# Kernel tuning notes

Hardware: AMD Instinct MI355X
Metric: run time of the kernel (lower is better)

## Reference

```python
import jax, jax.numpy as jnp
import numpy as np

B, T, E, H = 8, 1024, 1024, 16
HD = E // H  # head dim = 64
HID = 4 * E  # mlp hidden (stretch=4)
EPS = 1e-5


def setup_inputs() -> dict:
    key = jax.random.key(0)
    ks = jax.random.split(key, 8)
    s = lambda fan_in: 1.0 / np.sqrt(fan_in)
    return {
        "x": jax.random.normal(ks[0], (B, T, E), jnp.float32),
        # LayerNorm 1 (pre-attention)
        "ln1_g": jnp.ones((E,), jnp.float32),
        "ln1_b": jnp.zeros((E,), jnp.float32),
        # attention qkv + output proj (stored [in, out])
        "Wqkv": jax.random.normal(ks[1], (E, 3 * E), jnp.float32) * s(E),
        "bqkv": jnp.zeros((3 * E,), jnp.float32),
        "Wproj": jax.random.normal(ks[2], (E, E), jnp.float32) * s(E),
        "bproj": jnp.zeros((E,), jnp.float32),
        # LayerNorm 2 (pre-MLP)
        "ln2_g": jnp.ones((E,), jnp.float32),
        "ln2_b": jnp.zeros((E,), jnp.float32),
        # MLP: E -> 4E -> E with GELU
        "Wfc": jax.random.normal(ks[3], (E, HID), jnp.float32) * s(E),
        "bfc": jnp.zeros((HID,), jnp.float32),
        "Wout": jax.random.normal(ks[4], (HID, E), jnp.float32) * s(HID),
        "bout": jnp.zeros((E,), jnp.float32),
    }


def _layernorm(x, g, b):
    mu = jnp.mean(x, axis=-1, keepdims=True)
    var = jnp.mean(jnp.square(x - mu), axis=-1, keepdims=True)
    return (x - mu) * jax.lax.rsqrt(var + EPS) * g + b


def _attention(x, Wqkv, bqkv, Wproj, bproj):
    qkv = x @ Wqkv + bqkv                       # [B,T,3E]
    q, k, v = jnp.split(qkv, 3, axis=-1)
    # [B,T,E] -> [B,H,T,HD]
    rs = lambda t: t.reshape(B, T, H, HD).transpose(0, 2, 1, 3)
    q, k, v = rs(q), rs(k), rs(v)
    att = jnp.einsum("bhqd,bhkd->bhqk", q, k) * (1.0 / np.sqrt(HD))
    att = jax.nn.softmax(att, axis=-1)          # non-causal (BERT-style)
    y = jnp.einsum("bhqk,bhkd->bhqd", att, v)
    y = y.transpose(0, 2, 1, 3).reshape(B, T, E)
    return y @ Wproj + bproj


def reference(x, ln1_g, ln1_b, Wqkv, bqkv, Wproj, bproj,
              ln2_g, ln2_b, Wfc, bfc, Wout, bout):
    # res=1 => plain residual (w_att = w_mlp = 1.0); drop=0 => dropout identity
    x = x + _attention(_layernorm(x, ln1_g, ln1_b), Wqkv, bqkv, Wproj, bproj)
    h = _layernorm(x, ln2_g, ln2_b)
    x = x + (jax.nn.gelu(h @ Wfc + bfc) @ Wout + bout)
    return x
```

## Files before the change

kernel.cpp:

```cpp
#include <hip/hip_runtime.h>
#include <hip/hip_bf16.h>
#include <hip/hip_fp16.h>

#define B_   8
#define T_   1024
#define E_   1024
#define H_   16
#define HD_  64
#define HID_ 4096

typedef __attribute__((ext_vector_type(8))) _Float16 half8;
typedef __attribute__((ext_vector_type(4))) _Float16 half4;
typedef __attribute__((ext_vector_type(4))) float floatx4;

__device__ __forceinline__ float ld_in(const void* p, size_t i, int mode) {
    if (mode == 0) return ((const float*)p)[i];
    if (mode == 1) return (float)((const __hip_bfloat16*)p)[i];
    return (float)((const _Float16*)p)[i];
}
__device__ __forceinline__ void st_out(void* p, size_t i, int mode, float v) {
    if (mode == 0)      ((float*)p)[i] = v;
    else if (mode == 1) ((__hip_bfloat16*)p)[i] = (__hip_bfloat16)v;
    else                ((_Float16*)p)[i] = (_Float16)v;
}

__device__ __forceinline__ float gelu_f(float v) {
    return 0.5f * v * (1.0f + tanhf(0.7978845608028654f * (v + 0.044715f * v * v * v)));
}

__device__ __forceinline__ void gload_lds16(const void* g, void* l) {
    __builtin_amdgcn_global_load_lds(
        (const __attribute__((address_space(1))) void*)g,
        (__attribute__((address_space(3))) void*)l, 16, 0, 0);
}

__device__ __forceinline__ int xcd_remap(int orig, int nwg) {
    const int xcd = orig & 7, loc = orig >> 3;
    const int nq = nwg >> 3, rr = nwg & 7;
    return (xcd < rr ? xcd * (nq + 1) : rr * (nq + 1) + (xcd - rr) * nq) + loc;
}

__global__ void probe_mode(const void* __restrict__ g, int* __restrict__ mode) {
    if (threadIdx.x == 0) {
        unsigned u = *(const unsigned*)g;
        *mode = (u == 0x3F800000u) ? 0 : 1;
    }
}

__global__ __launch_bounds__(1024) void transpose_cvt(
    const void* __restrict__ in, _Float16* __restrict__ out, int K, int N,
    const int* __restrict__ modep)
{
    const int dm = *modep;
    __shared__ float t[32][33];
    const int n0 = blockIdx.x * 32, k0 = blockIdx.y * 32;
    t[threadIdx.y][threadIdx.x] =
        ld_in(in, (size_t)(k0 + threadIdx.y) * N + n0 + threadIdx.x, dm);
    __syncthreads();
    out[(size_t)(n0 + threadIdx.y) * K + k0 + threadIdx.x] = (_Float16)t[threadIdx.x][threadIdx.y];
}

__global__ __launch_bounds__(256) void ln_kernel(
    const void* __restrict__ x, size_t x_base,
    const void* __restrict__ g, const void* __restrict__ bta,
    _Float16* __restrict__ y, int xm_f, const int* __restrict__ modep)
{
    const int dm = *modep;
    const int xm = (xm_f >= 0) ? xm_f : dm;
    const size_t row = blockIdx.x;
    const int t = threadIdx.x;
    float v[4];
#pragma unroll
    for (int i = 0; i < 4; ++i) v[i] = ld_in(x, x_base + row * E_ + t * 4 + i, xm);
    float s = v[0] + v[1] + v[2] + v[3];
    float sq = v[0] * v[0] + v[1] * v[1] + v[2] * v[2] + v[3] * v[3];
#pragma unroll
    for (int off = 32; off; off >>= 1) { s += __shfl_xor(s, off); sq += __shfl_xor(sq, off); }
    __shared__ float sa[4], sb[4];
    const int wv = t >> 6, ln = t & 63;
    if (ln == 0) { sa[wv] = s; sb[wv] = sq; }
    __syncthreads();
    s  = sa[0] + sa[1] + sa[2] + sa[3];
    sq = sb[0] + sb[1] + sb[2] + sb[3];
    const float mu = s * (1.0f / E_);
    const float var = sq * (1.0f / E_) - mu * mu;
    const float rs = rsqrtf(var + 1e-5f);
#pragma unroll
    for (int i = 0; i < 4; ++i) {
        const int c = t * 4 + i;
        y[row * E_ + c] = (_Float16)(((v[i] - mu) * rs) * ld_in(g, c, dm) + ld_in(bta, c, dm));
    }
}

template <int ACT, int RES, int SPLIT>
__global__ __launch_bounds__(256) void gemm_bt(
    const _Float16* __restrict__ A, const _Float16* __restrict__ Bt,
    const void* __restrict__ bias, const void* __restrict__ resid, size_t r_base,
    void* __restrict__ C, size_t c_base, int M, int N, int K,
    int rm_f, int om_f, const int* __restrict__ modep,
    _Float16* __restrict__ qp, _Float16* __restrict__ kp, _Float16* __restrict__ vtp)
{
    const int dm = *modep;
    const int rm = (rm_f >= 0) ? rm_f : dm;
    const int om = (om_f >= 0) ? om_f : dm;
    __shared__ __align__(16) _Float16 As[128 * 32];
    __shared__ __align__(16) _Float16 Bs[128 * 32];
    const int tid = threadIdx.x;
    const int wave = tid >> 6, lane = tid & 63;
    const int wr = wave >> 1, wc = wave & 1;
    const int l15 = lane & 15, q = lane >> 4;
    const size_t row0 = (size_t)blockIdx.y * 128, col0 = (size_t)blockIdx.x * 128;
    const int srow = lane >> 2;
    const int skp = (lane & 3) * 8;
    floatx4 acc[4][4] = {};

    for (int k0 = 0; k0 < K; k0 += 32) {
#pragma unroll
        for (int tt = 0; tt < 2; ++tt) {
            const int c = wave * 2 + tt;
            gload_lds16(A  + (row0 + c * 16 + srow) * K + k0 + skp, As + c * 512);
            gload_lds16(Bt + (col0 + c * 16 + srow) * K + k0 + skp, Bs + c * 512);
        }
        __syncthreads();
        half8 af[4], bf[4];
#pragma unroll
        for (int i = 0; i < 4; ++i) {
            af[i] = *(const half8*)(As + (wr * 64 + i * 16 + l15) * 32 + q * 8);
            bf[i] = *(const half8*)(Bs + (wc * 64 + i * 16 + l15) * 32 + q * 8);
        }
#pragma unroll
        for (int i = 0; i < 4; ++i)
#pragma unroll
            for (int j = 0; j < 4; ++j)
                acc[i][j] = __builtin_amdgcn_mfma_f32_16x16x32_f16(af[i], bf[j], acc[i][j], 0, 0, 0);
        __syncthreads();
    }
#pragma unroll
    for (int i = 0; i < 4; ++i) {
#pragma unroll
        for (int j = 0; j < 4; ++j) {
            const size_t col = col0 + wc * 64 + j * 16 + l15;
            const float bv = ld_in(bias, col, dm);
#pragma unroll
            for (int r = 0; r < 4; ++r) {
                const size_t row = row0 + wr * 64 + i * 16 + q * 4 + r;
                float v = acc[i][j][r] + bv;
                if (ACT == 1) v = gelu_f(v);
                if (RES) v += ld_in(resid, r_base + row * N + col, rm);
                if (SPLIT) {
                    const int t = (int)row & 1023;
                    const size_t bh = ((row >> 10) << 4) + ((col >> 6) & 15);
                    const int part = (int)(col >> 10), hd = (int)col & 63;
                    const _Float16 hv = (_Float16)v;
                    if (part == 0)      qp[(bh * 1024 + t) * 64 + hd] = hv;
                    else if (part == 1) kp[(bh * 1024 + t) * 64 + hd] = hv;
                    else                vtp[(bh * 64 + hd) * 1024 + t] = hv;
                } else {
                    st_out(C, c_base + row * N + col, om, v);
                }
            }
        }
    }
}

#define PHASE256(MBASE, STAGE_STMT, TAIL_STMT)                                  \
    {                                                                           \
        half8 af[2][2];                                                         \
        _Pragma("unroll") for (int mi = 0; mi < 2; ++mi)                        \
            _Pragma("unroll") for (int ks = 0; ks < 2; ++ks)                    \
                af[mi][ks] = rdA(buf, (MBASE) + mi, ks);                        \
        STAGE_STMT;                                                             \
        __builtin_amdgcn_sched_barrier(0);                                      \
        __builtin_amdgcn_s_barrier();                                           \
        __builtin_amdgcn_sched_barrier(0);                                      \
        __builtin_amdgcn_s_setprio(1);                                          \
        _Pragma("unroll") for (int mi = 0; mi < 2; ++mi)                        \
            _Pragma("unroll") for (int n = 0; n < 4; ++n)                       \
                _Pragma("unroll") for (int ks = 0; ks < 2; ++ks)                \
                    acc[(MBASE) + mi][n] = __builtin_amdgcn_mfma_f32_16x16x32_f16( \
                        af[mi][ks], bf[n][ks], acc[(MBASE) + mi][n], 0, 0, 0);  \
        __builtin_amdgcn_s_setprio(0);                                          \
        TAIL_STMT;                                                              \
        __builtin_amdgcn_sched_barrier(0);                                      \
        __builtin_amdgcn_s_barrier();                                           \
    }

template <int ACT, int SPLIT>
__global__ __launch_bounds__(512, 2) void gemm256(
    const _Float16* __restrict__ A, const _Float16* __restrict__ Bt,
    const void* __restrict__ bias,
    void* __restrict__ C, size_t c_base, int M, int N, int K,
    int om_f, const int* __restrict__ modep,
    _Float16* __restrict__ qp, _Float16* __restrict__ kp, _Float16* __restrict__ vtp)
{
    (void)M;
    const int dm = __builtin_amdgcn_readfirstlane(*modep);
    const int om = (om_f >= 0) ? om_f : dm;
    __shared__ __align__(16) _Float16 lds[2][4][8192];
    const int tid = threadIdx.x;
    const int wave = tid >> 6, lane = tid & 63;
    const int l15 = lane & 15, q = lane >> 4;
    const int wr = wave >> 2, wc = wave & 3;
    const int nwg = (int)(gridDim.x * gridDim.y);
    const int wg = xcd_remap((int)(blockIdx.y * gridDim.x + blockIdx.x), nwg);
    const size_t row0 = (size_t)(wg / (int)gridDim.x) * 256;
    const size_t col0 = (size_t)(wg % (int)gridDim.x) * 256;
    const int NT = K >> 6;

    const int srow_in = lane >> 3;
    const int sch = lane & 7;

    auto stage = [&](int t, int h) {
        const int sbuf = t & 1;
        const int k0 = t << 6;
#pragma unroll
        for (int c = 0; c < 2; ++c) {
            const int seg = wave * 2 + c;
            const int row = seg * 8 + srow_in;
            const int ch = sch ^ (row & 7);
            const _Float16* src = (h < 2)
                ? A  + (size_t)(row0 + h * 128 + row) * K + k0 + ch * 8
                : Bt + (size_t)(col0 + (h - 2) * 128 + row) * K + k0 + ch * 8;
            gload_lds16(src, &lds[sbuf][h][seg * 512]);
        }
    };
    auto rdA = [&](int buf, int m, int ks) -> half8 {
        const int row = m * 16 + l15;
        const int ch = (ks * 4 + q) ^ (row & 7);
        return *(const half8*)(&lds[buf][wr][row * 64 + ch * 8]);
    };
    auto rdB = [&](int buf, int n, int ks) -> half8 {
        const int row = (wc & 1) * 64 + n * 16 + l15;
        const int ch = (ks * 4 + q) ^ (row & 7);
        return *(const half8*)(&lds[buf][2 + (wc >> 1)][row * 64 + ch * 8]);
    };

    floatx4 acc[8][4] = {};
    half8 bf[4][2];

    stage(0, 0); stage(0, 1); stage(0, 2); stage(0, 3);
    stage(1, 2); stage(1, 3);
    asm volatile("s_waitcnt vmcnt(4)" ::: "memory");
    __builtin_amdgcn_s_barrier();

    for (int u = 0; u < NT - 1; ++u) {
        const int buf = u & 1;
        {
#pragma unroll
            for (int n = 0; n < 4; ++n)
#pragma unroll
                for (int ks = 0; ks < 2; ++ks)
                    bf[n][ks] = rdB(buf, n, ks);
            PHASE256(0, { stage(u + 1, 0); stage(u + 1, 1); }, ;)
        }
        PHASE256(2, if (u + 2 < NT) stage(u + 2, 2), ;)
        PHASE256(4, if (u + 2 < NT) stage(u + 2, 3), ;)
        PHASE256(6, ;, asm volatile("s_waitcnt vmcnt(4)" ::: "memory"))
    }

    asm volatile("s_waitcnt vmcnt(0)" ::: "memory");
    __builtin_amdgcn_s_barrier();
    {
        const int buf = (NT - 1) & 1;
#pragma unroll
        for (int n = 0; n < 4; ++n)
#pragma unroll
            for (int ks = 0; ks < 2; ++ks)
                bf[n][ks] = rdB(buf, n, ks);
#pragma unroll
        for (int m = 0; m < 8; ++m) {
            half8 af2[2];
#pragma unroll
            for (int ks = 0; ks < 2; ++ks) af2[ks] = rdA(buf, m, ks);
#pragma unroll
            for (int n = 0; n < 4; ++n)
#pragma unroll
                for (int ks = 0; ks < 2; ++ks)
                    acc[m][n] = __builtin_amdgcn_mfma_f32_16x16x32_f16(af2[ks], bf[n][ks], acc[m][n], 0, 0, 0);
        }
    }

#pragma unroll
    for (int m = 0; m < 8; ++m) {
#pragma unroll
        for (int n = 0; n < 4; ++n) {
            const size_t col = col0 + wc * 64 + n * 16 + l15;
            const float bv = ld_in(bias, col, dm);
#pragma unroll
            for (int r = 0; r < 4; ++r) {
                const size_t row = row0 + wr * 128 + m * 16 + q * 4 + r;
                float v = acc[m][n][r] + bv;
                if (ACT == 1) v = gelu_f(v);
                if (SPLIT) {
                    const int t = (int)row & 1023;
                    const size_t bh = ((row >> 10) << 4) + ((col >> 6) & 15);
                    const int part = (int)(col >> 10), hd = (int)col & 63;
                    const _Float16 hv = (_Float16)v;
                    if (part == 0)      qp[(bh * 1024 + t) * 64 + hd] = hv;
                    else if (part == 1) kp[(bh * 1024 + t) * 64 + hd] = hv;
                    else                vtp[(bh * 64 + hd) * 1024 + t] = hv;
                } else {
                    st_out(C, c_base + row * N + col, om, v);
                }
            }
        }
    }
}
#undef PHASE256

template <int RES>
__global__ __launch_bounds__(512, 2) void gemm256n128(
    const _Float16* __restrict__ A, const _Float16* __restrict__ Bt,
    const void* __restrict__ bias, const void* __restrict__ resid, size_t r_base,
    void* __restrict__ C, size_t c_base, int M, int N, int K,
    int rm_f, int om_f, const int* __restrict__ modep)
{
    (void)M;
    const int dm = __builtin_amdgcn_readfirstlane(*modep);
    const int rm = (rm_f >= 0) ? rm_f : dm;
    const int om = (om_f >= 0) ? om_f : dm;
    __shared__ __align__(16) _Float16 lds[2][3][8192];
    const int tid = threadIdx.x;
    const int wave = tid >> 6, lane = tid & 63;
    const int l15 = lane & 15, q = lane >> 4;
    const int wr = wave >> 1, wc = wave & 1;
    const int nwg = (int)(gridDim.x * gridDim.y);
    const int wg = xcd_remap((int)(blockIdx.y * gridDim.x + blockIdx.x), nwg);
    const size_t row0 = (size_t)(wg / (int)gridDim.x) * 256;
    const size_t col0 = (size_t)(wg % (int)gridDim.x) * 128;
    const int NT = K >> 6;
    const int srow_in = lane >> 3;
    const int sch = lane & 7;

    auto stage = [&](int t, int h) {
        const int sbuf = t & 1;
        const int k0 = t << 6;
#pragma unroll
        for (int c = 0; c < 2; ++c) {
            const int seg = wave * 2 + c;
            const int row = seg * 8 + srow_in;
            const int ch = sch ^ (row & 7);
            const _Float16* src = (h < 2)
                ? A  + (size_t)(row0 + h * 128 + row) * K + k0 + ch * 8
                : Bt + (size_t)(col0 + row) * K + k0 + ch * 8;
            gload_lds16(src, &lds[sbuf][h][seg * 512]);
        }
    };
    auto rdA = [&](int buf, int m, int ks) -> half8 {
        const int gr = wr * 64 + m * 16 + l15;
        const int hf = gr >> 7, r = gr & 127;
        const int ch = (ks * 4 + q) ^ (r & 7);
        return *(const half8*)(&lds[buf][hf][r * 64 + ch * 8]);
    };
    auto rdB = [&](int buf, int n, int ks) -> half8 {
        const int r = wc * 64 + n * 16 + l15;
        const int ch = (ks * 4 + q) ^ (r & 7);
        return *(const half8*)(&lds[buf][2][r * 64 + ch * 8]);
    };

    floatx4 acc[4][4] = {};
    half8 bf[4][2];

    stage(0, 0); stage(0, 1); stage(0, 2);
    stage(1, 2);
    asm volatile("s_waitcnt vmcnt(2)" ::: "memory");
    __builtin_amdgcn_s_barrier();

    for (int u = 0; u < NT - 1; ++u) {
        const int buf = u & 1;
        {
            half8 af[2][2];
#pragma unroll
            for (int n = 0; n < 4; ++n)
#pragma unroll
                for (int ks = 0; ks < 2; ++ks)
                    bf[n][ks] = rdB(buf, n, ks);
#pragma unroll
            for (int mi = 0; mi < 2; ++mi)
#pragma unroll
                for (int ks = 0; ks < 2; ++ks)
                    af[mi][ks] = rdA(buf, mi, ks);
            stage(u + 1, 0); stage(u + 1, 1);
            __builtin_amdgcn_sched_barrier(0);
            __builtin_amdgcn_s_barrier();
            __builtin_amdgcn_sched_barrier(0);
            __builtin_amdgcn_s_setprio(1);
#pragma unroll
            for (int mi = 0; mi < 2; ++mi)
#pragma unroll
                for (int n = 0; n < 4; ++n)
#pragma unroll
                    for (int ks = 0; ks < 2; ++ks)
                        acc[mi][n] = __builtin_amdgcn_mfma_f32_16x16x32_f16(
                            af[mi][ks], bf[n][ks], acc[mi][n], 0, 0, 0);
            __builtin_amdgcn_s_setprio(0);
            __builtin_amdgcn_sched_barrier(0);
            __builtin_amdgcn_s_barrier();
        }
        {
            half8 af[2][2];
#pragma unroll
            for (int mi = 0; mi < 2; ++mi)
#pragma unroll
                for (int ks = 0; ks < 2; ++ks)
                    af[mi][ks] = rdA(buf, 2 + mi, ks);
            if (u + 2 < NT) stage(u + 2, 2);
            __builtin_amdgcn_sched_barrier(0);
            __builtin_amdgcn_s_barrier();
            __builtin_amdgcn_sched_barrier(0);
            __builtin_amdgcn_s_setprio(1);
#pragma unroll
            for (int mi = 0; mi < 2; ++mi)
#pragma unroll
                for (int n = 0; n < 4; ++n)
#pragma unroll
                    for (int ks = 0; ks < 2; ++ks)
                        acc[2 + mi][n] = __builtin_amdgcn_mfma_f32_16x16x32_f16(
                            af[mi][ks], bf[n][ks], acc[2 + mi][n], 0, 0, 0);
            __builtin_amdgcn_s_setprio(0);
            asm volatile("s_waitcnt vmcnt(2)" ::: "memory");
            __builtin_amdgcn_sched_barrier(0);
            __builtin_amdgcn_s_barrier();
        }
    }

    asm volatile("s_waitcnt vmcnt(0)" ::: "memory");
    __builtin_amdgcn_s_barrier();
    {
        const int buf = (NT - 1) & 1;
#pragma unroll
        for (int n = 0; n < 4; ++n)
#pragma unroll
            for (int ks = 0; ks < 2; ++ks)
                bf[n][ks] = rdB(buf, n, ks);
#pragma unroll
        for (int m = 0; m < 4; ++m) {
            half8 af2[2];
#pragma unroll
            for (int ks = 0; ks < 2; ++ks) af2[ks] = rdA(buf, m, ks);
#pragma unroll
            for (int n = 0; n < 4; ++n)
#pragma unroll
                for (int ks = 0; ks < 2; ++ks)
                    acc[m][n] = __builtin_amdgcn_mfma_f32_16x16x32_f16(
                        af2[ks], bf[n][ks], acc[m][n], 0, 0, 0);
        }
    }

#pragma unroll
    for (int m = 0; m < 4; ++m) {
#pragma unroll
        for (int n = 0; n < 4; ++n) {
            const size_t col = col0 + wc * 64 + n * 16 + l15;
            const float bv = ld_in(bias, col, dm);
#pragma unroll
            for (int r = 0; r < 4; ++r) {
                const size_t row = row0 + wr * 64 + m * 16 + q * 4 + r;
                float v = acc[m][n][r] + bv;
                if (RES) v += ld_in(resid, r_base + row * N + col, rm);
                st_out(C, c_base + row * N + col, om, v);
            }
        }
    }
}

template <int RES>
__global__ __launch_bounds__(256) void gemm_bt64(
    const _Float16* __restrict__ A, const _Float16* __restrict__ Bt,
    const void* __restrict__ bias, const void* __restrict__ resid, size_t r_base,
    void* __restrict__ C, size_t c_base, int M, int N, int K,
    int rm_f, int om_f, const int* __restrict__ modep)
{
    const int dm = *modep;
    const int rm = (rm_f >= 0) ? rm_f : dm;
    const int om = (om_f >= 0) ? om_f : dm;
    __shared__ __align__(16) _Float16 As[128 * 32];
    __shared__ __align__(16) _Float16 Bs[64 * 32];
    const int tid = threadIdx.x;
    const int wave = tid >> 6, lane = tid & 63;
    const int wr = wave >> 1, wc = wave & 1;
    const int l15 = lane & 15, q = lane >> 4;
    const size_t row0 = (size_t)blockIdx.y * 128, col0 = (size_t)blockIdx.x * 64;
    const int srow = lane >> 2;
    const int skp = (lane & 3) * 8;
    floatx4 acc[4][2] = {};

    for (int k0 = 0; k0 < K; k0 += 32) {
#pragma unroll
        for (int tt = 0; tt < 2; ++tt) {
            const int c = wave * 2 + tt;
            gload_lds16(A + (row0 + c * 16 + srow) * K + k0 + skp, As + c * 512);
        }
        gload_lds16(Bt + (col0 + wave * 16 + srow) * K + k0 + skp, Bs + wave * 512);
        __syncthreads();
        half8 af[4], bf[2];
#pragma unroll
        for (int i = 0; i < 4; ++i)
            af[i] = *(const half8*)(As + (wr * 64 + i * 16 + l15) * 32 + q * 8);
#pragma unroll
        for (int j = 0; j < 2; ++j)
            bf[j] = *(const half8*)(Bs + (wc * 32 + j * 16 + l15) * 32 + q * 8);
#pragma unroll
        for (int i = 0; i < 4; ++i)
#pragma unroll
            for (int j = 0; j < 2; ++j)
                acc[i][j] = __builtin_amdgcn_mfma_f32_16x16x32_f16(af[i], bf[j], acc[i][j], 0, 0, 0);
        __syncthreads();
    }
#pragma unroll
    for (int i = 0; i < 4; ++i) {
#pragma unroll
        for (int j = 0; j < 2; ++j) {
            const size_t col = col0 + wc * 32 + j * 16 + l15;
            const float bv = ld_in(bias, col, dm);
#pragma unroll
            for (int r = 0; r < 4; ++r) {
                const size_t row = row0 + wr * 64 + i * 16 + q * 4 + r;
                float v = acc[i][j][r] + bv;
                if (RES) v += ld_in(resid, r_base + row * N + col, rm);
                st_out(C, c_base + row * N + col, om, v);
            }
        }
    }
}

__global__ __launch_bounds__(256) void attn_mfma(
    const _Float16* __restrict__ Qh, const _Float16* __restrict__ Kh,
    const _Float16* __restrict__ Vt, _Float16* __restrict__ y)
{
    __shared__ __align__(16) _Float16 Ks[64 * 64];
    __shared__ __align__(16) _Float16 Vs[64 * 64];
    __shared__ __align__(16) _Float16 Pw[4][32][72];
    __shared__ float lw[4][32];
    const int tid = threadIdx.x, wave = tid >> 6, lane = tid & 63;
    const int l15 = lane & 15, q = lane >> 4;
    const int qt = blockIdx.x, bh = blockIdx.y;
    const int b = bh >> 4, h = bh & 15;
    const _Float16* Qb = Qh + (size_t)bh * 1024 * 64;
    const _Float16* Kb = Kh + (size_t)bh * 1024 * 64;
    const _Float16* Vb = Vt + (size_t)bh * 64 * 1024;

    half8 qf[2][2];
#pragma unroll
    for (int nt = 0; nt < 2; ++nt)
#pragma unroll
        for (int ks = 0; ks < 2; ++ks)
            qf[nt][ks] = *(const half8*)(Qb + (size_t)(qt * 128 + wave * 32 + nt * 16 + l15) * 64 + ks * 32 + q * 8);

    floatx4 oacc[2][4] = {};
    float lpart[2] = {0.f, 0.f};
    const int rl0 = wave * 16 + (lane >> 3);
    const int sseg = lane & 7;

    for (int kt = 0; kt < 16; ++kt) {
#pragma unroll
        for (int t = 0; t < 2; ++t) {
            const int rl = rl0 + t * 8;
            const int gs = sseg ^ (rl & 7);
            gload_lds16(Kb + (size_t)(kt * 64 + rl) * 64 + gs * 8, Ks + (wave * 16 + t * 8) * 64);
            gload_lds16(Vb + (size_t)rl * 1024 + kt * 64 + gs * 8, Vs + (wave * 16 + t * 8) * 64);
        }
        __syncthreads();

        floatx4 st[4][2] = {};
#pragma unroll
        for (int mt = 0; mt < 4; ++mt) {
            const int key = mt * 16 + l15;
#pragma unroll
            for (int ks = 0; ks < 2; ++ks) {
                const int s = (ks * 4 + q) ^ (key & 7);
                half8 kf = *(const half8*)(Ks + key * 64 + s * 8);
#pragma unroll
                for (int nt = 0; nt < 2; ++nt)
                    st[mt][nt] = __builtin_amdgcn_mfma_f32_16x16x32_f16(kf, qf[nt][ks], st[mt][nt], 0, 0, 0);
            }
        }
#pragma unroll
        for (int mt = 0; mt < 4; ++mt) {
#pragma unroll
            for (int nt = 0; nt < 2; ++nt) {
                float pv[4];
#pragma unroll
                for (int r = 0; r < 4; ++r) {
                    pv[r] = exp2f(st[mt][nt][r] * 0.18033688011112042f);
                    lpart[nt] += pv[r];
                }
                half4 h4 = {(_Float16)pv[0], (_Float16)pv[1], (_Float16)pv[2], (_Float16)pv[3]};
                *(half4*)(&Pw[wave][nt * 16 + l15][mt * 16 + q * 4]) = h4;
            }
        }
        asm volatile("s_waitcnt lgkmcnt(0)" ::: "memory");

#pragma unroll
        for (int ks = 0; ks < 2; ++ks) {
            half8 pf[2];
#pragma unroll
            for (int mt = 0; mt < 2; ++mt)
                pf[mt] = *(const half8*)(&Pw[wave][mt * 16 + l15][ks * 32 + q * 8]);
#pragma unroll
            for (int nt = 0; nt < 4; ++nt) {
                const int hd = nt * 16 + l15;
                const int s = (ks * 4 + q) ^ (hd & 7);
                half8 vf = *(const half8*)(Vs + hd * 64 + s * 8);
#pragma unroll
                for (int mt = 0; mt < 2; ++mt)
                    oacc[mt][nt] = __builtin_amdgcn_mfma_f32_16x16x32_f16(pf[mt], vf, oacc[mt][nt], 0, 0, 0);
            }
        }
        __syncthreads();
    }

#pragma unroll
    for (int nt = 0; nt < 2; ++nt) {
        lpart[nt] += __shfl_xor(lpart[nt], 16);
        lpart[nt] += __shfl_xor(lpart[nt], 32);
    }
    if (q == 0) { lw[wave][l15] = lpart[0]; lw[wave][16 + l15] = lpart[1]; }
    __syncthreads();

    const size_t ybase = (size_t)b * T_ * E_;
#pragma unroll
    for (int mt = 0; mt < 2; ++mt) {
        const floatx4 lv = *(const floatx4*)(&lw[wave][mt * 16 + q * 4]);
#pragma unroll
        for (int nt = 0; nt < 4; ++nt) {
            const int hd = nt * 16 + l15;
#pragma unroll
            for (int r = 0; r < 4; ++r) {
                const int t = qt * 128 + wave * 32 + mt * 16 + q * 4 + r;
                y[ybase + (size_t)t * E_ + h * 64 + hd] = (_Float16)(oacc[mt][nt][r] / lv[r]);
            }
        }
    }
}

extern "C" void kernel_launch(void* const* d_in, const int* in_sizes, int n_in,
                              void* d_out, int out_size, void* d_ws, size_t ws_size,
                              hipStream_t stream)
{
    const void* x     = d_in[0];
    const void* ln1_g = d_in[1];
    const void* ln1_b = d_in[2];
    const void* Wqkv  = d_in[3];
    const void* bqkv  = d_in[4];
    const void* Wproj = d_in[5];
    const void* bproj = d_in[6];
    const void* ln2_g = d_in[7];
    const void* ln2_b = d_in[8];
    const void* Wfc   = d_in[9];
    const void* bfc   = d_in[10];
    const void* Wout  = d_in[11];
    const void* bout  = d_in[12];

    const size_t MiB = 1ull << 20;
    int* modep = (int*)d_ws;
    char* base = (char*)d_ws + 4096;
    probe_mode<<<1, 64, 0, stream>>>(ln1_g, modep);

    dim3 tb(32, 32);

    if (ws_size >= 96 * MiB + 4096) {
        _Float16* Qh      = (_Float16*)(base);
        _Float16* Kh      = (_Float16*)(base + 16 * MiB);
        _Float16* Vt      = (_Float16*)(base + 32 * MiB);
        _Float16* Wt_qkv  = (_Float16*)(base + 48 * MiB);
        _Float16* lnc     = (_Float16*)(base + 56 * MiB);
        _Float16* x1      = (_Float16*)(base);
        _Float16* Wt_fc   = (_Float16*)(base + 16 * MiB);
        _Float16* Wt_out  = (_Float16*)(base + 24 * MiB);
        _Float16* Wt_proj = (_Float16*)(base + 48 * MiB);
        _Float16* hact    = (_Float16*)(base + 32 * MiB);
        _Float16* ybuf    = (_Float16*)d_out;
        _Float16* ln2buf  = (_Float16*)d_out;

        transpose_cvt<<<dim3(96, 32), tb, 0, stream>>>(Wqkv, Wt_qkv, E_, 3 * E_, modep);
        ln_kernel<<<8192, 256, 0, stream>>>(x, 0, ln1_g, ln1_b, lnc, -1, modep);
        gemm256<0, 1><<<dim3(12, 32), 512, 0, stream>>>(
            lnc, Wt_qkv, bqkv, nullptr, 0, 8192, 3 * E_, E_, 2, modep,
            Qh, Kh, Vt);
        attn_mfma<<<dim3(8, B_ * H_), 256, 0, stream>>>(Qh, Kh, Vt, ybuf);

        transpose_cvt<<<dim3(32, 32), tb, 0, stream>>>(Wproj, Wt_proj, E_, E_, modep);
        gemm256n128<1><<<dim3(8, 32), 512, 0, stream>>>(
            ybuf, Wt_proj, bproj, x, 0, x1, 0, B_ * T_, E_, E_, -1, 2, modep);

        transpose_cvt<<<dim3(128, 32), tb, 0, stream>>>(Wfc, Wt_fc, E_, HID_, modep);
        transpose_cvt<<<dim3(32, 128), tb, 0, stream>>>(Wout, Wt_out, HID_, E_, modep);
        ln_kernel<<<8192, 256, 0, stream>>>(x1, 0, ln2_g, ln2_b, ln2buf, 2, modep);
        gemm256<1, 0><<<dim3(16, 32), 512, 0, stream>>>(
            ln2buf, Wt_fc, bfc, hact, 0, 8192, HID_, E_, 2, modep,
            nullptr, nullptr, nullptr);
        gemm256n128<1><<<dim3(8, 32), 512, 0, stream>>>(
            hact, Wt_out, bout, x1, 0, d_out, 0, 8192, E_, HID_, 2, -1, modep);
    } else if (ws_size >= 64 * MiB + 4096) {
        _Float16* Qh      = (_Float16*)(base);
        _Float16* Kh      = (_Float16*)(base + 16 * MiB);
        _Float16* Vt      = (_Float16*)(base + 32 * MiB);
        _Float16* Wt_qkv  = (_Float16*)(base + 48 * MiB);
        _Float16* lnc     = (_Float16*)(base + 54 * MiB);
        _Float16* x1      = (_Float16*)(base);
        _Float16* Wt_fc   = (_Float16*)(base + 16 * MiB);
        _Float16* Wt_out  = (_Float16*)(base + 24 * MiB);
        _Float16* Wt_proj = (_Float16*)(base + 48 * MiB);
        _Float16* hact    = (_Float16*)(base + 32 * MiB);
        _Float16* ybuf    = (_Float16*)d_out;
        _Float16* ln2buf  = (_Float16*)d_out;

        transpose_cvt<<<dim3(96, 32), tb, 0, stream>>>(Wqkv, Wt_qkv, E_, 3 * E_, modep);
        for (int c = 0; c < 2; ++c) {
            const size_t ro = (size_t)c * 4096;
            ln_kernel<<<4096, 256, 0, stream>>>(x, ro * E_, ln1_g, ln1_b, lnc, -1, modep);
            const size_t po = ro * 1024;
            gemm256<0, 1><<<dim3(12, 16), 512, 0, stream>>>(
                lnc, Wt_qkv, bqkv, nullptr, 0, 4096, 3 * E_, E_, 2, modep,
                Qh + po, Kh + po, Vt + po);
        }
        attn_mfma<<<dim3(8, B_ * H_), 256, 0, stream>>>(Qh, Kh, Vt, ybuf);

        transpose_cvt<<<dim3(32, 32), tb, 0, stream>>>(Wproj, Wt_proj, E_, E_, modep);
        gemm256n128<1><<<dim3(8, 32), 512, 0, stream>>>(
            ybuf, Wt_proj, bproj, x, 0, x1, 0, B_ * T_, E_, E_, -1, 2, modep);

        transpose_cvt<<<dim3(128, 32), tb, 0, stream>>>(Wfc, Wt_fc, E_, HID_, modep);
        transpose_cvt<<<dim3(32, 128), tb, 0, stream>>>(Wout, Wt_out, HID_, E_, modep);
        ln_kernel<<<8192, 256, 0, stream>>>(x1, 0, ln2_g, ln2_b, ln2buf, 2, modep);
        for (int c = 1; c >= 0; --c) {
            const size_t off = (size_t)c * 4096 * E_;
            gemm256<1, 0><<<dim3(16, 16), 512, 0, stream>>>(
                ln2buf + off, Wt_fc, bfc, hact, 0, 4096, HID_, E_, 2, modep,
                nullptr, nullptr, nullptr);
            gemm256n128<1><<<dim3(8, 16), 512, 0, stream>>>(
                hact, Wt_out, bout, x1 + off, 0, d_out, off, 4096, E_, HID_, 2, -1, modep);
        }
    } else {
        _Float16* Wt_qkv  = (_Float16*)(base);
        _Float16* Wt_proj = (_Float16*)(base + 6 * MiB);
        _Float16* L       = (_Float16*)(base + 8 * MiB);
        _Float16* Qc      = (_Float16*)(base + 10 * MiB);
        _Float16* Kc      = (_Float16*)(base + 12 * MiB);
        _Float16* Vc      = (_Float16*)(base + 14 * MiB);
        _Float16* Y       = (_Float16*)(base + 16 * MiB);
        _Float16* Wt_fc   = (_Float16*)(base);
        _Float16* Wt_out  = (_Float16*)(base + 8 * MiB);
        _Float16* L2      = (_Float16*)(base + 16 * MiB);
        _Float16* hact    = (_Float16*)(base + 18 * MiB);

        transpose_cvt<<<dim3(96, 32), tb, 0, stream>>>(Wqkv, Wt_qkv, E_, 3 * E_, modep);
        transpose_cvt<<<dim3(32, 32), tb, 0, stream>>>(Wproj, Wt_proj, E_, E_, modep);

        for (int b = 0; b < B_; ++b) {
            const size_t boff = (size_t)b * T_ * E_;
            ln_kernel<<<T_, 256, 0, stream>>>(x, boff, ln1_g, ln1_b, L, -1, modep);
            gemm_bt<0, 0, 1><<<dim3(24, 8), 256, 0, stream>>>(
                L, Wt_qkv, bqkv, nullptr, 0, nullptr, 0, T_, 3 * E_, E_, 2, 2, modep,
                Qc, Kc, Vc);
            attn_mfma<<<dim3(8, H_), 256, 0, stream>>>(Qc, Kc, Vc, Y);
            gemm_bt64<1><<<dim3(16, 8), 256, 0, stream>>>(
                Y, Wt_proj, bproj, x, boff, d_out, boff, T_, E_, E_, -1, -1, modep);
        }

        transpose_cvt<<<dim3(128, 32), tb, 0, stream>>>(Wfc, Wt_fc, E_, HID_, modep);
        transpose_cvt<<<dim3(32, 128), tb, 0, stream>>>(Wout, Wt_out, HID_, E_, modep);

        for (int c = 0; c < 8; ++c) {
            const size_t off = (size_t)c * 1024 * E_;
            ln_kernel<<<1024, 256, 0, stream>>>(d_out, off, ln2_g, ln2_b, L2, -1, modep);
            gemm_bt<1, 0, 0><<<dim3(32, 8), 256, 0, stream>>>(
                L2, Wt_fc, bfc, nullptr, 0, hact, 0, 1024, HID_, E_, 2, 2, modep,
                nullptr, nullptr, nullptr);
            gemm_bt64<1><<<dim3(16, 8), 256, 0, stream>>>(
                hact, Wt_out, bout, d_out, off, d_out, off, 1024, E_, HID_, -1, -1, modep);
        }
    }
}
```

Baseline: 649.2 us.

## Make FC GEMM persistent over two row tiles and use exp-based GELU

Adds a PERSIST template parameter so each gemm256 workgroup handles several row tiles in sequence. The first k-tiles of the next tile are prefetched during the previous tile's final MFMA and epilogue. The FC1 GEMM now launches 256 workgroups that each cover two row tiles, which hides the prologue and epilogue latency and drops the tail wave. GELU's tanhf is replaced by an algebraically equivalent __expf form, which is cheaper but may lose precision or overflow to inf for large inputs.

```diff
diff --git a/kernel.cpp b/kernel.cpp
--- a/kernel.cpp
+++ b/kernel.cpp
@@ -25,7 +25,9 @@
 }
 
 __device__ __forceinline__ float gelu_f(float v) {
-    return 0.5f * v * (1.0f + tanhf(0.7978845608028654f * (v + 0.044715f * v * v * v)));
+    const float u = 0.7978845608028654f * (v + 0.044715f * v * v * v);
+    const float t = __expf(2.0f * u);
+    return v - v / (t + 1.0f);
 }
 
 __device__ __forceinline__ void gload_lds16(const void* g, void* l) {
@@ -185,7 +187,7 @@
         __builtin_amdgcn_s_barrier();                                           \
     }
 
-template <int ACT, int SPLIT>
+template <int ACT, int SPLIT, int PERSIST>
 __global__ __launch_bounds__(512, 2) void gemm256(
     const _Float16* __restrict__ A, const _Float16* __restrict__ Bt,
     const void* __restrict__ bias,
@@ -203,14 +205,15 @@
     const int wr = wave >> 2, wc = wave & 3;
     const int nwg = (int)(gridDim.x * gridDim.y);
     const int wg = xcd_remap((int)(blockIdx.y * gridDim.x + blockIdx.x), nwg);
-    const size_t row0 = (size_t)(wg / (int)gridDim.x) * 256;
+    const size_t rowbase = (size_t)(wg / (int)gridDim.x) * 256;
+    const size_t rowstep = (size_t)gridDim.y * 256;
     const size_t col0 = (size_t)(wg % (int)gridDim.x) * 256;
     const int NT = K >> 6;
 
     const int srow_in = lane >> 3;
     const int sch = lane & 7;
 
-    auto stage = [&](int t, int h) {
+    auto stage = [&](size_t r0, int t, int h) {
         const int sbuf = t & 1;
         const int k0 = t << 6;
 #pragma unroll
@@ -219,7 +222,7 @@
             const int row = seg * 8 + srow_in;
             const int ch = sch ^ (row & 7);
             const _Float16* src = (h < 2)
-                ? A  + (size_t)(row0 + h * 128 + row) * K + k0 + ch * 8
+                ? A  + (size_t)(r0 + h * 128 + row) * K + k0 + ch * 8
                 : Bt + (size_t)(col0 + (h - 2) * 128 + row) * K + k0 + ch * 8;
             gload_lds16(src, &lds[sbuf][h][seg * 512]);
         }
@@ -235,74 +238,89 @@
         return *(const half8*)(&lds[buf][2 + (wc >> 1)][row * 64 + ch * 8]);
     };
 
-    floatx4 acc[8][4] = {};
-    half8 bf[4][2];
-
-    stage(0, 0); stage(0, 1); stage(0, 2); stage(0, 3);
-    stage(1, 2); stage(1, 3);
+    stage(rowbase, 0, 0); stage(rowbase, 0, 1); stage(rowbase, 0, 2); stage(rowbase, 0, 3);
+    stage(rowbase, 1, 2); stage(rowbase, 1, 3);
     asm volatile("s_waitcnt vmcnt(4)" ::: "memory");
     __builtin_amdgcn_s_barrier();
 
-    for (int u = 0; u < NT - 1; ++u) {
-        const int buf = u & 1;
+#pragma unroll 1
+    for (int half = 0; half < PERSIST; ++half) {
+        const size_t row0 = rowbase + (size_t)half * rowstep;
+        floatx4 acc[8][4] = {};
+        half8 bf[4][2];
+
+        for (int u = 0; u < NT - 1; ++u) {
+            const int buf = u & 1;
+            {
+#pragma unroll
+                for (int n = 0; n < 4; ++n)
+#pragma unroll
+                    for (int ks = 0; ks < 2; ++ks)
+                        bf[n][ks] = rdB(buf, n, ks);
+                PHASE256(0, { stage(row0, u + 1, 0); stage(row0, u + 1, 1); }, ;)
+            }
+            PHASE256(2, if (u + 2 < NT) stage(row0, u + 2, 2), ;)
+            PHASE256(4, if (u + 2 < NT) stage(row0, u + 2, 3), ;)
+            PHASE256(6, ;, asm volatile("s_waitcnt vmcnt(4)" ::: "memory"))
+        }
+
+        asm volatile("s_waitcnt vmcnt(0)" ::: "memory");
+        __builtin_amdgcn_s_barrier();
+        const size_t nrow0 = row0 + rowstep;
+        if (half + 1 < PERSIST) {
+            stage(nrow0, 0, 0); stage(nrow0, 0, 1); stage(nrow0, 0, 2); stage(nrow0, 0, 3);
+        }
         {
+            const int buf = (NT - 1) & 1;
 #pragma unroll
             for (int n = 0; n < 4; ++n)
 #pragma unroll
                 for (int ks = 0; ks < 2; ++ks)
                     bf[n][ks] = rdB(buf, n, ks);
-            PHASE256(0, { stage(u + 1, 0); stage(u + 1, 1); }, ;)
-        }
-        PHASE256(2, if (u + 2 < NT) stage(u + 2, 2), ;)
-        PHASE256(4, if (u + 2 < NT) stage(u + 2, 3), ;)
-        PHASE256(6, ;, asm volatile("s_waitcnt vmcnt(4)" ::: "memory"))
-    }
-
-    asm volatile("s_waitcnt vmcnt(0)" ::: "memory");
-    __builtin_amdgcn_s_barrier();
-    {
-        const int buf = (NT - 1) & 1;
-#pragma unroll
-        for (int n = 0; n < 4; ++n)
-#pragma unroll
-            for (int ks = 0; ks < 2; ++ks)
-                bf[n][ks] = rdB(buf, n, ks);
+#pragma unroll
+            for (int m = 0; m < 8; ++m) {
+                half8 af2[2];
+#pragma unroll
+                for (int ks = 0; ks < 2; ++ks) af2[ks] = rdA(buf, m, ks);
+#pragma unroll
+                for (int n = 0; n < 4; ++n)
+#pragma unroll
+                    for (int ks = 0; ks < 2; ++ks)
+                        acc[m][n] = __builtin_amdgcn_mfma_f32_16x16x32_f16(af2[ks], bf[n][ks], acc[m][n], 0, 0, 0);
+            }
+        }
+
 #pragma unroll
         for (int m = 0; m < 8; ++m) {
-            half8 af2[2];
-#pragma unroll
-            for (int ks = 0; ks < 2; ++ks) af2[ks] = rdA(buf, m, ks);
-#pragma unroll
-            for (int n = 0; n < 4; ++n)
-#pragma unroll
-                for (int ks = 0; ks < 2; ++ks)
-                    acc[m][n] = __builtin_amdgcn_mfma_f32_16x16x32_f16(af2[ks], bf[n][ks], acc[m][n], 0, 0, 0);
-        }
-    }
-
-#pragma unroll
-    for (int m = 0; m < 8; ++m) {
-#pragma unroll
-        for (int n = 0; n < 4; ++n) {
-            const size_t col = col0 + wc * 64 + n * 16 + l15;
-            const float bv = ld_in(bias, col, dm);
-#pragma unroll
-            for (int r = 0; r < 4; ++r) {
-                const size_t row = row0 + wr * 128 + m * 16 + q * 4 + r;
-                float v = acc[m][n][r] + bv;
-                if (ACT == 1) v = gelu_f(v);
-                if (SPLIT) {
-                    const int t = (int)row & 1023;
-                    const size_t bh = ((row >> 10) << 4) + ((col >> 6) & 15);
-                    const int part = (int)(col >> 10), hd = (int)col & 63;
-                    const _Float16 hv = (_Float16)v;
-                    if (part == 0)      qp[(bh * 1024 + t) * 64 + hd] = hv;
-                    else if (part == 1) kp[(bh * 1024 + t) * 64 + hd] = hv;
-                    else                vtp[(bh * 64 + hd) * 1024 + t] = hv;
-                } else {
-                    st_out(C, c_base + row * N + col, om, v);
+#pragma unroll
+            for (int n = 0; n < 4; ++n) {
+                const size_t col = col0 + wc * 64 + n * 16 + l15;
+                const float bv = ld_in(bias, col, dm);
+#pragma unroll
+                for (int r = 0; r < 4; ++r) {
+                    const size_t row = row0 + wr * 128 + m * 16 + q * 4 + r;
+                    float v = acc[m][n][r] + bv;
+                    if (ACT == 1) v = gelu_f(v);
+                    if (SPLIT) {
+                        const int t = (int)row & 1023;
+                        const size_t bh = ((row >> 10) << 4) + ((col >> 6) & 15);
+                        const int part = (int)(col >> 10), hd = (int)col & 63;
+                        const _Float16 hv = (_Float16)v;
+                        if (part == 0)      qp[(bh * 1024 + t) * 64 + hd] = hv;
+                        else if (part == 1) kp[(bh * 1024 + t) * 64 + hd] = hv;
+                        else                vtp[(bh * 64 + hd) * 1024 + t] = hv;
+                    } else {
+                        st_out(C, c_base + row * N + col, om, v);
+                    }
                 }
             }
+        }
+
+        if (half + 1 < PERSIST) {
+            __builtin_amdgcn_s_barrier();
+            stage(nrow0, 1, 2); stage(nrow0, 1, 3);
+            asm volatile("s_waitcnt vmcnt(4)" ::: "memory");
+            __builtin_amdgcn_s_barrier();
         }
     }
 }
@@ -675,7 +693,7 @@
 
         transpose_cvt<<<dim3(96, 32), tb, 0, stream>>>(Wqkv, Wt_qkv, E_, 3 * E_, modep);
         ln_kernel<<<8192, 256, 0, stream>>>(x, 0, ln1_g, ln1_b, lnc, -1, modep);
-        gemm256<0, 1><<<dim3(12, 32), 512, 0, stream>>>(
+        gemm256<0, 1, 1><<<dim3(12, 32), 512, 0, stream>>>(
             lnc, Wt_qkv, bqkv, nullptr, 0, 8192, 3 * E_, E_, 2, modep,
             Qh, Kh, Vt);
         attn_mfma<<<dim3(8, B_ * H_), 256, 0, stream>>>(Qh, Kh, Vt, ybuf);
@@ -687,7 +705,7 @@
         transpose_cvt<<<dim3(128, 32), tb, 0, stream>>>(Wfc, Wt_fc, E_, HID_, modep);
         transpose_cvt<<<dim3(32, 128), tb, 0, stream>>>(Wout, Wt_out, HID_, E_, modep);
         ln_kernel<<<8192, 256, 0, stream>>>(x1, 0, ln2_g, ln2_b, ln2buf, 2, modep);
-        gemm256<1, 0><<<dim3(16, 32), 512, 0, stream>>>(
+        gemm256<1, 0, 2><<<dim3(16, 16), 512, 0, stream>>>(
             ln2buf, Wt_fc, bfc, hact, 0, 8192, HID_, E_, 2, modep,
             nullptr, nullptr, nullptr);
         gemm256n128<1><<<dim3(8, 32), 512, 0, stream>>>(
@@ -711,7 +729,7 @@
             const size_t ro = (size_t)c * 4096;
             ln_kernel<<<4096, 256, 0, stream>>>(x, ro * E_, ln1_g, ln1_b, lnc, -1, modep);
             const size_t po = ro * 1024;
-            gemm256<0, 1><<<dim3(12, 16), 512, 0, stream>>>(
+            gemm256<0, 1, 1><<<dim3(12, 16), 512, 0, stream>>>(
                 lnc, Wt_qkv, bqkv, nullptr, 0, 4096, 3 * E_, E_, 2, modep,
                 Qh + po, Kh + po, Vt + po);
         }
@@ -726,7 +744,7 @@
         ln_kernel<<<8192, 256, 0, stream>>>(x1, 0, ln2_g, ln2_b, ln2buf, 2, modep);
         for (int c = 1; c >= 0; --c) {
             const size_t off = (size_t)c * 4096 * E_;
-            gemm256<1, 0><<<dim3(16, 16), 512, 0, stream>>>(
+            gemm256<1, 0, 1><<<dim3(16, 16), 512, 0, stream>>>(
                 ln2buf + off, Wt_fc, bfc, hact, 0, 4096, HID_, E_, 2, modep,
                 nullptr, nullptr, nullptr);
             gemm256n128<1><<<dim3(8, 16), 512, 0, stream>>>(
```

Result: faster. 612.8 us (-5.6%).
